# Kernel tuning notes

Hardware: AMD Instinct MI355X
Metric: run time of the kernel (lower is better)

## Reference

```python
import jax, jax.numpy as jnp
import numpy as np

N_PATCHES = 16
HID = 8
HEADS = 2
DH = HID // HEADS          # 4
L = 2                       # n_blocks
DIM = 10                    # betas.shape[0]
C = 3
S_DIM = 224
PS = S_DIM // N_PATCHES     # 14
INPUT_D = C * PS * PS       # 588
SEQ = N_PATCHES ** 2 + 1    # 257
MLP = 4 * HID               # 32
EPS = 1e-5


def _pos_embed():
    i = np.arange(SEQ, dtype=np.float64)[:, None]
    j = np.arange(HID, dtype=np.float64)[None, :]
    ang = i / 10000.0 ** ((j - (j % 2)) / HID)
    pe = np.where(j % 2 == 0, np.sin(ang), np.cos(ang))
    return jnp.asarray(pe, jnp.float32)


def setup_inputs() -> dict:
    key = jax.random.key(0)
    ks = jax.random.split(key, 24)
    g = lambda k, shape: (jax.random.normal(k, shape, jnp.float32) * 0.1)
    inp = {
        'images': jax.random.normal(ks[0], (512, C, S_DIM, S_DIM), jnp.float32),
        'inputs_labels': jax.random.randint(ks[1], (512,), 0, C),
        'Wm': g(ks[2], (INPUT_D, HID)), 'bm': g(ks[3], (HID,)),
        'cls_table': g(ks[4], (C, HID)),
        'pe': _pos_embed(),
        'ln1_g': jnp.ones((L, HID)), 'ln1_b': jnp.zeros((L, HID)),
        'Wq': g(ks[5], (L, HEADS, DH, DH)), 'bq': g(ks[6], (L, HEADS, DH)),
        'Wk': g(ks[7], (L, HEADS, DH, DH)), 'bk': g(ks[8], (L, HEADS, DH)),
        'Wv': g(ks[9], (L, HEADS, DH, DH)), 'bv': g(ks[10], (L, HEADS, DH)),
        'ln2_g': jnp.ones((L, HID)), 'ln2_b': jnp.zeros((L, HID)),
        'W1': g(ks[11], (L, HID, MLP)), 'b1': g(ks[12], (L, MLP)),
        'W2': g(ks[13], (L, MLP, HID)), 'b2': g(ks[14], (L, HID)),
        'Wf': g(ks[15], (HID, DIM)), 'bf': g(ks[16], (DIM,)),
    }
    return inp


def _layernorm(x, g, b):
    m = jnp.mean(x, axis=-1, keepdims=True)
    v = jnp.mean(jnp.square(x - m), axis=-1, keepdims=True)
    return (x - m) * jax.lax.rsqrt(v + EPS) * g + b


def _forward(images, inputs_labels, Wm, bm, cls_table, pe,
             ln1_g, ln1_b, Wq, bq, Wk, bk, Wv, bv,
             ln2_g, ln2_b, W1, b1, W2, b2, Wf, bf):
    n = images.shape[0]
    # patchify: [n,C,H,W] -> [n, n_patches^2, C*ps*ps]
    p = images.reshape(n, C, N_PATCHES, PS, N_PATCHES, PS)
    p = p.transpose(0, 2, 4, 1, 3, 5).reshape(n, N_PATCHES ** 2, INPUT_D)
    tokens = p @ Wm + bm                                # [n, 256, HID]
    cls = cls_table[inputs_labels][:, None, :]          # [n, 1, HID]
    x = jnp.concatenate([cls, tokens], axis=1) + pe[None]  # [n, SEQ, HID]
    scale = 1.0 / jnp.sqrt(jnp.float32(DH))
    for l in range(L):
        h = _layernorm(x, ln1_g[l], ln1_b[l]).reshape(n, SEQ, HEADS, DH)
        q = jnp.einsum('nshd,hde->nhse', h, Wq[l]) + bq[l][None, :, None, :]
        k = jnp.einsum('nshd,hde->nhse', h, Wk[l]) + bk[l][None, :, None, :]
        v = jnp.einsum('nshd,hde->nhse', h, Wv[l]) + bv[l][None, :, None, :]
        att = jax.nn.softmax(jnp.einsum('nhse,nhte->nhst', q, k) * scale, axis=-1)
        o = jnp.einsum('nhst,nhte->nhse', att, v)       # [n,H,S,DH]
        x = x + o.transpose(0, 2, 1, 3).reshape(n, SEQ, HID)
        h2 = _layernorm(x, ln2_g[l], ln2_b[l])
        x = x + jax.nn.gelu(h2 @ W1[l] + b1[l], approximate=False) @ W2[l] + b2[l]
    return x[:, 0] @ Wf + bf                            # [n, DIM]


def reference(images, inputs_labels, Wm, bm, cls_table, pe,
              ln1_g, ln1_b, Wq, bq, Wk, bk, Wv, bv,
              ln2_g, ln2_b, W1, b1, W2, b2, Wf, bf):
    return _forward(images, inputs_labels, Wm, bm, cls_table, pe,
                    ln1_g, ln1_b, Wq, bq, Wk, bk, Wv, bv,
                    ln2_g, ln2_b, W1, b1, W2, b2, Wf, bf)
```

## Files before the change

### kernel.cpp

```cpp
#include <hip/hip_runtime.h>

#define N_IMG_D 150528
#define CH_STRIDE 50176

__global__ __launch_bounds__(256) void k_patch_embed(
    const float* __restrict__ img, const float* __restrict__ Wm,
    const float* __restrict__ bm, const float* __restrict__ pe,
    float* __restrict__ xws)
{
    __shared__ __align__(16) float wmA[588 * 4];
    __shared__ __align__(16) float wmB[588 * 4];
    __shared__ __align__(16) float red[224 * 8];

    const int t = threadIdx.x;
    const int b = blockIdx.x;
    const int n = b >> 4, py = b & 15;

    for (int i = t; i < 1176; i += 256) {
        float4 w = reinterpret_cast<const float4*>(Wm)[i];
        float* dst = (i & 1) ? wmB : wmA;
        *reinterpret_cast<float4*>(dst + (i >> 1) * 4) = w;
    }
    __syncthreads();

    if (t < 224) {
        const int rp = t / 112;
        const int t1 = t - rp * 112;
        const int px = t1 / 7;
        const int j  = t1 - px * 7;
        const int col0 = 2 * j;
        const float* ib = img + (size_t)n * N_IMG_D + (py * 14) * 224 + px * 14 + col0;
        float a0=0,a1=0,a2=0,a3=0,a4=0,a5=0,a6=0,a7=0;
        int c = 0, r = rp;
        const float* wA = wmA + (rp * 14 + col0) * 4;
        const float* wB = wmB + (rp * 14 + col0) * 4;
        #pragma unroll
        for (int it = 0; it < 21; ++it) {
            const float2 v = *reinterpret_cast<const float2*>(ib + c * CH_STRIDE + r * 224);
            const float4 wa0 = *reinterpret_cast<const float4*>(wA);
            const float4 wa1 = *reinterpret_cast<const float4*>(wA + 4);
            const float4 wb0 = *reinterpret_cast<const float4*>(wB);
            const float4 wb1 = *reinterpret_cast<const float4*>(wB + 4);
            a0 += v.x * wa0.x + v.y * wa1.x;
            a1 += v.x * wa0.y + v.y * wa1.y;
            a2 += v.x * wa0.z + v.y * wa1.z;
            a3 += v.x * wa0.w + v.y * wa1.w;
            a4 += v.x * wb0.x + v.y * wb1.x;
            a5 += v.x * wb0.y + v.y * wb1.y;
            a6 += v.x * wb0.z + v.y * wb1.z;
            a7 += v.x * wb0.w + v.y * wb1.w;
            r += 2;
            if (r >= 14) { r -= 14; c += 1; }
            wA += 28 * 4; wB += 28 * 4;
        }
        *reinterpret_cast<float4*>(red + t * 8)     = make_float4(a0, a1, a2, a3);
        *reinterpret_cast<float4*>(red + t * 8 + 4) = make_float4(a4, a5, a6, a7);
    }
    __syncthreads();

    if (t < 128) {
        const int px = t >> 3, e = t & 7;
        float s = 0.f;
        #pragma unroll
        for (int rp = 0; rp < 2; ++rp) {
            #pragma unroll
            for (int j = 0; j < 7; ++j)
                s += red[(rp * 112 + px * 7 + j) * 8 + e];
        }
        const int row = 1 + py * 16 + px;
        s += bm[e] + pe[row * 8 + e];
        xws[((size_t)n * 257 + row) * 8 + e] = s;
    }
}

__global__ __launch_bounds__(576) void k_transformer(
    const float* __restrict__ xws, const int* __restrict__ labels,
    const float* __restrict__ cls_table, const float* __restrict__ pe,
    const float* __restrict__ ln1_g, const float* __restrict__ ln1_b,
    const float* __restrict__ Wq, const float* __restrict__ bq,
    const float* __restrict__ Wk, const float* __restrict__ bk,
    const float* __restrict__ Wv, const float* __restrict__ bv,
    const float* __restrict__ ln2_g, const float* __restrict__ ln2_b,
    const float* __restrict__ W1, const float* __restrict__ b1,
    const float* __restrict__ W2, const float* __restrict__ b2,
    const float* __restrict__ Wf, const float* __restrict__ bf,
    float* __restrict__ out)
{
    __shared__ __align__(16) float xb[257 * 9];
    __shared__ __align__(16) float hb[257 * 9];
    __shared__ __align__(16) float qb[2 * 257 * 4];
    __shared__ __align__(16) float kb[2 * 257 * 4];
    __shared__ __align__(16) float vb[2 * 257 * 4];
    __shared__ float wqs[64], wks[64], wvs[64];
    __shared__ float bqs[16], bks[16], bvs[16];
    __shared__ float w1s[512], b1s[64], w2s[512], b2s[16];

    const int t = threadIdx.x;
    const int n = blockIdx.x;
    const float* xn = xws + (size_t)n * 2056;

    for (int i = t; i < 64; i += 576) { wqs[i] = Wq[i]; wks[i] = Wk[i]; wvs[i] = Wv[i]; b1s[i] = b1[i]; }
    for (int i = t; i < 16; i += 576) { bqs[i] = bq[i]; bks[i] = bk[i]; bvs[i] = bv[i]; b2s[i] = b2[i]; }
    for (int i = t; i < 512; i += 576) { w1s[i] = W1[i]; w2s[i] = W2[i]; }

    if (t < 512) {
        float4 v = reinterpret_cast<const float4*>(xn)[t + 2];
        const int s = (t + 2) >> 1;
        const int e0 = (t & 1) ? 4 : 0;
        float* d = xb + s * 9 + e0;
        d[0] = v.x; d[1] = v.y; d[2] = v.z; d[3] = v.w;
    } else if (t < 520) {
        const int e = t - 512;
        xb[e] = cls_table[labels[n] * 8 + e] + pe[e];
    }
    __syncthreads();

    const float SC = 0.72134752044f;

    for (int l = 0; l < 2; ++l) {
        if (t < 257) {
            float v0[8]; float m = 0.f;
            #pragma unroll
            for (int e = 0; e < 8; ++e) { v0[e] = xb[t * 9 + e]; m += v0[e]; }
            m *= 0.125f;
            float var = 0.f;
            #pragma unroll
            for (int e = 0; e < 8; ++e) { float d = v0[e] - m; var += d * d; }
            var *= 0.125f;
            const float rs = rsqrtf(var + 1e-5f);
            const float* g = ln1_g + l * 8; const float* bb = ln1_b + l * 8;
            float ln[8];
            #pragma unroll
            for (int e = 0; e < 8; ++e) ln[e] = (v0[e] - m) * rs * g[e] + bb[e];

            #pragma unroll
            for (int h = 0; h < 2; ++h) {
                const int wb_ = (l * 2 + h);
                const float* wq = wqs + wb_ * 16; const float* bq_ = bqs + wb_ * 4;
                const float* wk = wks + wb_ * 16; const float* bk_ = bks + wb_ * 4;
                const float* wv = wvs + wb_ * 16; const float* bv_ = bvs + wb_ * 4;
                float qq[4], kk[4], vv[4];
                #pragma unroll
                for (int e = 0; e < 4; ++e) { qq[e] = bq_[e]; kk[e] = bk_[e]; vv[e] = bv_[e]; }
                #pragma unroll
                for (int d = 0; d < 4; ++d) {
                    const float hd = ln[h * 4 + d];
                    #pragma unroll
                    for (int e = 0; e < 4; ++e) {
                        qq[e] += hd * wq[d * 4 + e];
                        kk[e] += hd * wk[d * 4 + e];
                        vv[e] += hd * wv[d * 4 + e];
                    }
                }
                const int ri = (h * 257 + t) * 4;
                *reinterpret_cast<float4*>(qb + ri) =
                    make_float4(qq[0] * SC, qq[1] * SC, qq[2] * SC, qq[3] * SC);
                *reinterpret_cast<float4*>(kb + ri) = make_float4(kk[0], kk[1], kk[2], kk[3]);
                *reinterpret_cast<float4*>(vb + ri) = make_float4(vv[0], vv[1], vv[2], vv[3]);
            }
        }
        __syncthreads();

        if (t < 258) {
            const int h = (t >= 129) ? 1 : 0;
            const int j = t - 129 * h;
            const int s0 = j;
            const int s1 = j + 129;
            const bool has2 = (j < 128);
            const float4* qp = reinterpret_cast<const float4*>(qb) + h * 257;
            const float4* kp = reinterpret_cast<const float4*>(kb) + h * 257;
            const float4* vp = reinterpret_cast<const float4*>(vb) + h * 257;
            const float4 q0 = qp[s0];
            const float4 q1 = qp[has2 ? s1 : s0];

            float l0 = 0.f, o00 = 0.f, o01 = 0.f, o02 = 0.f, o03 = 0.f;
            float l1 = 0.f, o10 = 0.f, o11 = 0.f, o12 = 0.f, o13 = 0.f;
            #pragma unroll 4
            for (int tt = 0; tt < 257; ++tt) {
                const float4 kk = kp[tt];
                const float4 vv = vp[tt];
                const float d0 = q0.x * kk.x + q0.y * kk.y + q0.z * kk.z + q0.w * kk.w;
                const float d1 = q1.x * kk.x + q1.y * kk.y + q1.z * kk.z + q1.w * kk.w;
                const float p0 = exp2f(d0);
                const float p1 = exp2f(d1);
                l0 += p0; l1 += p1;
                o00 += p0 * vv.x; o01 += p0 * vv.y; o02 += p0 * vv.z; o03 += p0 * vv.w;
                o10 += p1 * vv.x; o11 += p1 * vv.y; o12 += p1 * vv.z; o13 += p1 * vv.w;
            }
            const float i0 = 1.0f / l0;
            float* xr0 = xb + s0 * 9 + h * 4;
            xr0[0] += o00 * i0; xr0[1] += o01 * i0; xr0[2] += o02 * i0; xr0[3] += o03 * i0;
            if (has2) {
                const float i1 = 1.0f / l1;
                float* xr1 = xb + s1 * 9 + h * 4;
                xr1[0] += o10 * i1; xr1[1] += o11 * i1; xr1[2] += o12 * i1; xr1[3] += o13 * i1;
            }
        }
        __syncthreads();

        if (t < 257) {
            float v0[8]; float m = 0.f;
            #pragma unroll
            for (int e = 0; e < 8; ++e) { v0[e] = xb[t * 9 + e]; m += v0[e]; }
            m *= 0.125f;
            float var = 0.f;
            #pragma unroll
            for (int e = 0; e < 8; ++e) { float d = v0[e] - m; var += d * d; }
            var *= 0.125f;
            const float rs = rsqrtf(var + 1e-5f);
            const float* g = ln2_g + l * 8; const float* bb = ln2_b + l * 8;
            #pragma unroll
            for (int e = 0; e < 8; ++e) hb[t * 9 + e] = (v0[e] - m) * rs * g[e] + bb[e];
        }
        __syncthreads();

        if (t < 257) {
            float hv[8];
            #pragma unroll
            for (int e = 0; e < 8; ++e) hv[e] = hb[t * 9 + e];
            float acc[8] = {0.f, 0.f, 0.f, 0.f, 0.f, 0.f, 0.f, 0.f};
            const float* w1 = w1s + l * 256; const float* bb1 = b1s + l * 32;
            const float* w2 = w2s + l * 256; const float* bb2 = b2s + l * 8;
            for (int u = 0; u < 32; ++u) {
                float a = bb1[u];
                #pragma unroll
                for (int e = 0; e < 8; ++e) a += hv[e] * w1[e * 32 + u];
                const float gl = 0.5f * a * (1.0f + erff(a * 0.70710678f));
                #pragma unroll
                for (int e = 0; e < 8; ++e) acc[e] += gl * w2[u * 8 + e];
            }
            #pragma unroll
            for (int e = 0; e < 8; ++e) xb[t * 9 + e] += acc[e] + bb2[e];
        }
        __syncthreads();
    }

    if (t < 10) {
        float a = bf[t];
        #pragma unroll
        for (int e = 0; e < 8; ++e) a += xb[e] * Wf[e * 10 + t];
        out[(size_t)n * 10 + t] = a;
    }
}

extern "C" void kernel_launch(void* const* d_in, const int* in_sizes, int n_in,
                              void* d_out, int out_size, void* d_ws, size_t ws_size,
                              hipStream_t stream) {
    const float* img    = (const float*)d_in[0];
    const int*   labels = (const int*)  d_in[1];
    const float* Wm     = (const float*)d_in[2];
    const float* bm     = (const float*)d_in[3];
    const float* cls    = (const float*)d_in[4];
    const float* pe     = (const float*)d_in[5];
    const float* ln1_g  = (const float*)d_in[6];
    const float* ln1_b  = (const float*)d_in[7];
    const float* Wq     = (const float*)d_in[8];
    const float* bq     = (const float*)d_in[9];
    const float* Wk     = (const float*)d_in[10];
    const float* bk     = (const float*)d_in[11];
    const float* Wv     = (const float*)d_in[12];
    const float* bv     = (const float*)d_in[13];
    const float* ln2_g  = (const float*)d_in[14];
    const float* ln2_b  = (const float*)d_in[15];
    const float* W1     = (const float*)d_in[16];
    const float* b1     = (const float*)d_in[17];
    const float* W2     = (const float*)d_in[18];
    const float* b2     = (const float*)d_in[19];
    const float* Wf     = (const float*)d_in[20];
    const float* bf     = (const float*)d_in[21];
    float* out = (float*)d_out;
    float* xws = (float*)d_ws;

    const int n = in_sizes[0] / N_IMG_D;
    k_patch_embed<<<n * 16, 256, 0, stream>>>(img, Wm, bm, pe, xws);
    k_transformer<<<n, 576, 0, stream>>>(xws, labels, cls, pe, ln1_g, ln1_b,
        Wq, bq, Wk, bk, Wv, bv, ln2_g, ln2_b, W1, b1, W2, b2, Wf, bf, out);
}
```

Baseline: 564.8 us.

## Fuse patch embedding into transformer kernel and retile attention to four queries per thread

Removes the separate patch-embedding kernel. Each transformer block now computes its own patch tokens: 512 threads each handle one patch and one half of the 21 rows, reading Wm directly from global memory, and the two halves are combined through shared memory. This drops the workspace round trip and one kernel launch. Attention is also remapped so 128 threads each process four queries, plus two threads for the last row, which reuses each K/V load across more queries but runs on far fewer active threads. The per-thread image reads in the fused embedding are strided, and with only 512 blocks the image-loading phase may be less well parallelised than the earlier 8192-block kernel.

```diff
diff --git a/kernel.cpp b/kernel.cpp
--- a/kernel.cpp
+++ b/kernel.cpp
@@ -3,78 +3,9 @@
 #define N_IMG_D 150528
 #define CH_STRIDE 50176
 
-__global__ __launch_bounds__(256) void k_patch_embed(
-    const float* __restrict__ img, const float* __restrict__ Wm,
-    const float* __restrict__ bm, const float* __restrict__ pe,
-    float* __restrict__ xws)
-{
-    __shared__ __align__(16) float wmA[588 * 4];
-    __shared__ __align__(16) float wmB[588 * 4];
-    __shared__ __align__(16) float red[224 * 8];
-
-    const int t = threadIdx.x;
-    const int b = blockIdx.x;
-    const int n = b >> 4, py = b & 15;
-
-    for (int i = t; i < 1176; i += 256) {
-        float4 w = reinterpret_cast<const float4*>(Wm)[i];
-        float* dst = (i & 1) ? wmB : wmA;
-        *reinterpret_cast<float4*>(dst + (i >> 1) * 4) = w;
-    }
-    __syncthreads();
-
-    if (t < 224) {
-        const int rp = t / 112;
-        const int t1 = t - rp * 112;
-        const int px = t1 / 7;
-        const int j  = t1 - px * 7;
-        const int col0 = 2 * j;
-        const float* ib = img + (size_t)n * N_IMG_D + (py * 14) * 224 + px * 14 + col0;
-        float a0=0,a1=0,a2=0,a3=0,a4=0,a5=0,a6=0,a7=0;
-        int c = 0, r = rp;
-        const float* wA = wmA + (rp * 14 + col0) * 4;
-        const float* wB = wmB + (rp * 14 + col0) * 4;
-        #pragma unroll
-        for (int it = 0; it < 21; ++it) {
-            const float2 v = *reinterpret_cast<const float2*>(ib + c * CH_STRIDE + r * 224);
-            const float4 wa0 = *reinterpret_cast<const float4*>(wA);
-            const float4 wa1 = *reinterpret_cast<const float4*>(wA + 4);
-            const float4 wb0 = *reinterpret_cast<const float4*>(wB);
-            const float4 wb1 = *reinterpret_cast<const float4*>(wB + 4);
-            a0 += v.x * wa0.x + v.y * wa1.x;
-            a1 += v.x * wa0.y + v.y * wa1.y;
-            a2 += v.x * wa0.z + v.y * wa1.z;
-            a3 += v.x * wa0.w + v.y * wa1.w;
-            a4 += v.x * wb0.x + v.y * wb1.x;
-            a5 += v.x * wb0.y + v.y * wb1.y;
-            a6 += v.x * wb0.z + v.y * wb1.z;
-            a7 += v.x * wb0.w + v.y * wb1.w;
-            r += 2;
-            if (r >= 14) { r -= 14; c += 1; }
-            wA += 28 * 4; wB += 28 * 4;
-        }
-        *reinterpret_cast<float4*>(red + t * 8)     = make_float4(a0, a1, a2, a3);
-        *reinterpret_cast<float4*>(red + t * 8 + 4) = make_float4(a4, a5, a6, a7);
-    }
-    __syncthreads();
-
-    if (t < 128) {
-        const int px = t >> 3, e = t & 7;
-        float s = 0.f;
-        #pragma unroll
-        for (int rp = 0; rp < 2; ++rp) {
-            #pragma unroll
-            for (int j = 0; j < 7; ++j)
-                s += red[(rp * 112 + px * 7 + j) * 8 + e];
-        }
-        const int row = 1 + py * 16 + px;
-        s += bm[e] + pe[row * 8 + e];
-        xws[((size_t)n * 257 + row) * 8 + e] = s;
-    }
-}
-
-__global__ __launch_bounds__(576) void k_transformer(
-    const float* __restrict__ xws, const int* __restrict__ labels,
+__global__ __launch_bounds__(576) void k_vit_fused(
+    const float* __restrict__ img, const int* __restrict__ labels,
+    const float* __restrict__ Wm, const float* __restrict__ bm,
     const float* __restrict__ cls_table, const float* __restrict__ pe,
     const float* __restrict__ ln1_g, const float* __restrict__ ln1_b,
     const float* __restrict__ Wq, const float* __restrict__ bq,
@@ -91,27 +22,54 @@
     __shared__ __align__(16) float qb[2 * 257 * 4];
     __shared__ __align__(16) float kb[2 * 257 * 4];
     __shared__ __align__(16) float vb[2 * 257 * 4];
+    __shared__ float red2[256 * 9];
     __shared__ float wqs[64], wks[64], wvs[64];
     __shared__ float bqs[16], bks[16], bvs[16];
     __shared__ float w1s[512], b1s[64], w2s[512], b2s[16];
 
     const int t = threadIdx.x;
     const int n = blockIdx.x;
-    const float* xn = xws + (size_t)n * 2056;
 
     for (int i = t; i < 64; i += 576) { wqs[i] = Wq[i]; wks[i] = Wk[i]; wvs[i] = Wv[i]; b1s[i] = b1[i]; }
     for (int i = t; i < 16; i += 576) { bqs[i] = bq[i]; bks[i] = bk[i]; bvs[i] = bv[i]; b2s[i] = b2[i]; }
     for (int i = t; i < 512; i += 576) { w1s[i] = W1[i]; w2s[i] = W2[i]; }
 
-    if (t < 512) {
-        float4 v = reinterpret_cast<const float4*>(xn)[t + 2];
-        const int s = (t + 2) >> 1;
-        const int e0 = (t & 1) ? 4 : 0;
-        float* d = xb + s * 9 + e0;
-        d[0] = v.x; d[1] = v.y; d[2] = v.z; d[3] = v.w;
+    const bool emb = (t < 512);
+    int half = 0, p = 0;
+    float acc[8] = {0.f, 0.f, 0.f, 0.f, 0.f, 0.f, 0.f, 0.f};
+    if (emb) {
+        half = __builtin_amdgcn_readfirstlane(t >> 8);
+        p = t & 255;
+        const int py = p >> 4, px = p & 15;
+        int c = half;
+        int r = half * 7;
+        const float* ib = img + (size_t)n * N_IMG_D + c * CH_STRIDE + (py * 14 + r) * 224 + px * 14;
+        const float* wrow = Wm + (c * 196 + r * 14) * 8;
+        for (int it = 0; it < 21; ++it) {
+            #pragma unroll 7
+            for (int col = 0; col < 14; ++col) {
+                const float v = ib[col];
+                const float* w = wrow + col * 8;
+                #pragma unroll
+                for (int e = 0; e < 8; ++e) acc[e] += v * w[e];
+            }
+            ++r; ib += 224; wrow += 112;
+            if (r == 14) { r = 0; ++c; ib += CH_STRIDE - 14 * 224; }
+        }
+        if (half) {
+            #pragma unroll
+            for (int e = 0; e < 8; ++e) red2[p * 9 + e] = acc[e];
+        }
     } else if (t < 520) {
         const int e = t - 512;
         xb[e] = cls_table[labels[n] * 8 + e] + pe[e];
+    }
+    __syncthreads();
+    if (emb && half == 0) {
+        const float* pr = pe + (p + 1) * 8;
+        #pragma unroll
+        for (int e = 0; e < 8; ++e)
+            xb[(p + 1) * 9 + e] = acc[e] + red2[p * 9 + e] + bm[e] + pr[e];
     }
     __syncthreads();
 
@@ -161,39 +119,65 @@
         }
         __syncthreads();
 
-        if (t < 258) {
-            const int h = (t >= 129) ? 1 : 0;
-            const int j = t - 129 * h;
-            const int s0 = j;
-            const int s1 = j + 129;
-            const bool has2 = (j < 128);
-            const float4* qp = reinterpret_cast<const float4*>(qb) + h * 257;
-            const float4* kp = reinterpret_cast<const float4*>(kb) + h * 257;
-            const float4* vp = reinterpret_cast<const float4*>(vb) + h * 257;
-            const float4 q0 = qp[s0];
-            const float4 q1 = qp[has2 ? s1 : s0];
-
-            float l0 = 0.f, o00 = 0.f, o01 = 0.f, o02 = 0.f, o03 = 0.f;
-            float l1 = 0.f, o10 = 0.f, o11 = 0.f, o12 = 0.f, o13 = 0.f;
-            #pragma unroll 4
-            for (int tt = 0; tt < 257; ++tt) {
-                const float4 kk = kp[tt];
-                const float4 vv = vp[tt];
-                const float d0 = q0.x * kk.x + q0.y * kk.y + q0.z * kk.z + q0.w * kk.w;
-                const float d1 = q1.x * kk.x + q1.y * kk.y + q1.z * kk.z + q1.w * kk.w;
-                const float p0 = exp2f(d0);
-                const float p1 = exp2f(d1);
-                l0 += p0; l1 += p1;
-                o00 += p0 * vv.x; o01 += p0 * vv.y; o02 += p0 * vv.z; o03 += p0 * vv.w;
-                o10 += p1 * vv.x; o11 += p1 * vv.y; o12 += p1 * vv.z; o13 += p1 * vv.w;
-            }
-            const float i0 = 1.0f / l0;
-            float* xr0 = xb + s0 * 9 + h * 4;
-            xr0[0] += o00 * i0; xr0[1] += o01 * i0; xr0[2] += o02 * i0; xr0[3] += o03 * i0;
-            if (has2) {
-                const float i1 = 1.0f / l1;
-                float* xr1 = xb + s1 * 9 + h * 4;
-                xr1[0] += o10 * i1; xr1[1] += o11 * i1; xr1[2] += o12 * i1; xr1[3] += o13 * i1;
+        if (t < 130) {
+            if (t < 128) {
+                const int h  = t >> 6;
+                const int j0 = t & 63;
+                const float4* qp = reinterpret_cast<const float4*>(qb) + h * 257;
+                const float4* kp = reinterpret_cast<const float4*>(kb) + h * 257;
+                const float4* vp = reinterpret_cast<const float4*>(vb) + h * 257;
+                const float4 q0 = qp[j0], q1 = qp[j0 + 64], q2 = qp[j0 + 128], q3 = qp[j0 + 192];
+                float l0 = 0.f, l1 = 0.f, l2 = 0.f, l3 = 0.f;
+                float4 o0 = {0,0,0,0}, o1 = {0,0,0,0}, o2 = {0,0,0,0}, o3 = {0,0,0,0};
+                #pragma unroll 2
+                for (int tt = 0; tt < 257; ++tt) {
+                    const float4 kk = kp[tt];
+                    const float4 vv = vp[tt];
+                    const float d0 = q0.x*kk.x + q0.y*kk.y + q0.z*kk.z + q0.w*kk.w;
+                    const float d1 = q1.x*kk.x + q1.y*kk.y + q1.z*kk.z + q1.w*kk.w;
+                    const float d2 = q2.x*kk.x + q2.y*kk.y + q2.z*kk.z + q2.w*kk.w;
+                    const float d3 = q3.x*kk.x + q3.y*kk.y + q3.z*kk.z + q3.w*kk.w;
+                    const float p0 = exp2f(d0), p1 = exp2f(d1), p2 = exp2f(d2), p3 = exp2f(d3);
+                    l0 += p0; l1 += p1; l2 += p2; l3 += p3;
+                    o0.x += p0*vv.x; o0.y += p0*vv.y; o0.z += p0*vv.z; o0.w += p0*vv.w;
+                    o1.x += p1*vv.x; o1.y += p1*vv.y; o1.z += p1*vv.z; o1.w += p1*vv.w;
+                    o2.x += p2*vv.x; o2.y += p2*vv.y; o2.z += p2*vv.z; o2.w += p2*vv.w;
+                    o3.x += p3*vv.x; o3.y += p3*vv.y; o3.z += p3*vv.z; o3.w += p3*vv.w;
+                }
+                {
+                    const float i0 = 1.0f / l0; float* xr = xb + (j0      ) * 9 + h * 4;
+                    xr[0] += o0.x*i0; xr[1] += o0.y*i0; xr[2] += o0.z*i0; xr[3] += o0.w*i0;
+                }
+                {
+                    const float i1 = 1.0f / l1; float* xr = xb + (j0 +  64) * 9 + h * 4;
+                    xr[0] += o1.x*i1; xr[1] += o1.y*i1; xr[2] += o1.z*i1; xr[3] += o1.w*i1;
+                }
+                {
+                    const float i2 = 1.0f / l2; float* xr = xb + (j0 + 128) * 9 + h * 4;
+                    xr[0] += o2.x*i2; xr[1] += o2.y*i2; xr[2] += o2.z*i2; xr[3] += o2.w*i2;
+                }
+                {
+                    const float i3 = 1.0f / l3; float* xr = xb + (j0 + 192) * 9 + h * 4;
+                    xr[0] += o3.x*i3; xr[1] += o3.y*i3; xr[2] += o3.z*i3; xr[3] += o3.w*i3;
+                }
+            } else {
+                const int h = t - 128;
+                const float4* qp = reinterpret_cast<const float4*>(qb) + h * 257;
+                const float4* kp = reinterpret_cast<const float4*>(kb) + h * 257;
+                const float4* vp = reinterpret_cast<const float4*>(vb) + h * 257;
+                const float4 q0 = qp[256];
+                float l0 = 0.f; float4 o0 = {0,0,0,0};
+                #pragma unroll 2
+                for (int tt = 0; tt < 257; ++tt) {
+                    const float4 kk = kp[tt];
+                    const float4 vv = vp[tt];
+                    const float d0 = q0.x*kk.x + q0.y*kk.y + q0.z*kk.z + q0.w*kk.w;
+                    const float p0 = exp2f(d0);
+                    l0 += p0;
+                    o0.x += p0*vv.x; o0.y += p0*vv.y; o0.z += p0*vv.z; o0.w += p0*vv.w;
+                }
+                const float i0 = 1.0f / l0; float* xr = xb + 256 * 9 + h * 4;
+                xr[0] += o0.x*i0; xr[1] += o0.y*i0; xr[2] += o0.z*i0; xr[3] += o0.w*i0;
             }
         }
         __syncthreads();
@@ -218,7 +202,7 @@
             float hv[8];
             #pragma unroll
             for (int e = 0; e < 8; ++e) hv[e] = hb[t * 9 + e];
-            float acc[8] = {0.f, 0.f, 0.f, 0.f, 0.f, 0.f, 0.f, 0.f};
+            float a8[8] = {0.f, 0.f, 0.f, 0.f, 0.f, 0.f, 0.f, 0.f};
             const float* w1 = w1s + l * 256; const float* bb1 = b1s + l * 32;
             const float* w2 = w2s + l * 256; const float* bb2 = b2s + l * 8;
             for (int u = 0; u < 32; ++u) {
@@ -227,10 +211,10 @@
                 for (int e = 0; e < 8; ++e) a += hv[e] * w1[e * 32 + u];
                 const float gl = 0.5f * a * (1.0f + erff(a * 0.70710678f));
                 #pragma unroll
-                for (int e = 0; e < 8; ++e) acc[e] += gl * w2[u * 8 + e];
-            }
-            #pragma unroll
-            for (int e = 0; e < 8; ++e) xb[t * 9 + e] += acc[e] + bb2[e];
+                for (int e = 0; e < 8; ++e) a8[e] += gl * w2[u * 8 + e];
+            }
+            #pragma unroll
+            for (int e = 0; e < 8; ++e) xb[t * 9 + e] += a8[e] + bb2[e];
         }
         __syncthreads();
     }
@@ -269,10 +253,9 @@
     const float* Wf     = (const float*)d_in[20];
     const float* bf     = (const float*)d_in[21];
     float* out = (float*)d_out;
-    float* xws = (float*)d_ws;
 
     const int n = in_sizes[0] / N_IMG_D;
-    k_patch_embed<<<n * 16, 256, 0, stream>>>(img, Wm, bm, pe, xws);
-    k_transformer<<<n, 576, 0, stream>>>(xws, labels, cls, pe, ln1_g, ln1_b,
-        Wq, bq, Wk, bk, Wv, bv, ln2_g, ln2_b, W1, b1, W2, b2, Wf, bf, out);
+    k_vit_fused<<<n, 576, 0, stream>>>(img, labels, Wm, bm, cls, pe,
+        ln1_g, ln1_b, Wq, bq, Wk, bk, Wv, bv, ln2_g, ln2_b,
+        W1, b1, W2, b2, Wf, bf, out);
 }
```

After: 630.0 us. 1.12x slower.

## Reuse patch-embed weight loads across four patches per thread

Applied to the files above, without the earlier changes.

The patch-embed kernel now has each thread cover the same column pair of four horizontally adjacent patches, so every shared-memory weight float4 load feeds four image float2 loads. Each thread keeps 32 accumulators and walks rows with a stride of 8 instead of 2. The reduction now sums 56 partials per output through a padded 33-stride shared buffer. This is meant to cut LDS weight traffic and raise memory-level parallelism on image reads, at the cost of more registers, a larger shared reduction buffer and an uneven split of 6 or 5 iterations across threads. The transformer-kernel edits are cosmetic only.

```diff
diff --git a/kernel.cpp b/kernel.cpp
--- a/kernel.cpp
+++ b/kernel.cpp
@@ -10,7 +10,7 @@
 {
     __shared__ __align__(16) float wmA[588 * 4];
     __shared__ __align__(16) float wmB[588 * 4];
-    __shared__ __align__(16) float red[224 * 8];
+    __shared__ float red[224 * 33];
 
     const int t = threadIdx.x;
     const int b = blockIdx.x;
@@ -24,52 +24,65 @@
     __syncthreads();
 
     if (t < 224) {
-        const int rp = t / 112;
-        const int t1 = t - rp * 112;
-        const int px = t1 / 7;
-        const int j  = t1 - px * 7;
+        const int s   = t / 28;
+        const int t1  = t - s * 28;
+        const int pg4 = t1 / 7;
+        const int j   = t1 - pg4 * 7;
         const int col0 = 2 * j;
-        const float* ib = img + (size_t)n * N_IMG_D + (py * 14) * 224 + px * 14 + col0;
-        float a0=0,a1=0,a2=0,a3=0,a4=0,a5=0,a6=0,a7=0;
-        int c = 0, r = rp;
-        const float* wA = wmA + (rp * 14 + col0) * 4;
-        const float* wB = wmB + (rp * 14 + col0) * 4;
-        #pragma unroll
-        for (int it = 0; it < 21; ++it) {
-            const float2 v = *reinterpret_cast<const float2*>(ib + c * CH_STRIDE + r * 224);
+        int c = 0, r = s;
+        const float* ib = img + (size_t)n * N_IMG_D + (py * 14 + r) * 224 + pg4 * 14 + col0;
+        const float* wA = wmA + (s * 14 + col0) * 4;
+        const float* wB = wmB + (s * 14 + col0) * 4;
+        float a[32];
+        #pragma unroll
+        for (int i = 0; i < 32; ++i) a[i] = 0.f;
+        const int iters = (s < 2) ? 6 : 5;
+        for (int it = 0; it < iters; ++it) {
+            const float2 v0 = *reinterpret_cast<const float2*>(ib);
+            const float2 v1 = *reinterpret_cast<const float2*>(ib + 56);
+            const float2 v2 = *reinterpret_cast<const float2*>(ib + 112);
+            const float2 v3 = *reinterpret_cast<const float2*>(ib + 168);
             const float4 wa0 = *reinterpret_cast<const float4*>(wA);
             const float4 wa1 = *reinterpret_cast<const float4*>(wA + 4);
             const float4 wb0 = *reinterpret_cast<const float4*>(wB);
             const float4 wb1 = *reinterpret_cast<const float4*>(wB + 4);
-            a0 += v.x * wa0.x + v.y * wa1.x;
-            a1 += v.x * wa0.y + v.y * wa1.y;
-            a2 += v.x * wa0.z + v.y * wa1.z;
-            a3 += v.x * wa0.w + v.y * wa1.w;
-            a4 += v.x * wb0.x + v.y * wb1.x;
-            a5 += v.x * wb0.y + v.y * wb1.y;
-            a6 += v.x * wb0.z + v.y * wb1.z;
-            a7 += v.x * wb0.w + v.y * wb1.w;
-            r += 2;
-            if (r >= 14) { r -= 14; c += 1; }
-            wA += 28 * 4; wB += 28 * 4;
-        }
-        *reinterpret_cast<float4*>(red + t * 8)     = make_float4(a0, a1, a2, a3);
-        *reinterpret_cast<float4*>(red + t * 8 + 4) = make_float4(a4, a5, a6, a7);
+            a[0]  += v0.x*wa0.x + v0.y*wa1.x;  a[1]  += v0.x*wa0.y + v0.y*wa1.y;
+            a[2]  += v0.x*wa0.z + v0.y*wa1.z;  a[3]  += v0.x*wa0.w + v0.y*wa1.w;
+            a[4]  += v0.x*wb0.x + v0.y*wb1.x;  a[5]  += v0.x*wb0.y + v0.y*wb1.y;
+            a[6]  += v0.x*wb0.z + v0.y*wb1.z;  a[7]  += v0.x*wb0.w + v0.y*wb1.w;
+            a[8]  += v1.x*wa0.x + v1.y*wa1.x;  a[9]  += v1.x*wa0.y + v1.y*wa1.y;
+            a[10] += v1.x*wa0.z + v1.y*wa1.z;  a[11] += v1.x*wa0.w + v1.y*wa1.w;
+            a[12] += v1.x*wb0.x + v1.y*wb1.x;  a[13] += v1.x*wb0.y + v1.y*wb1.y;
+            a[14] += v1.x*wb0.z + v1.y*wb1.z;  a[15] += v1.x*wb0.w + v1.y*wb1.w;
+            a[16] += v2.x*wa0.x + v2.y*wa1.x;  a[17] += v2.x*wa0.y + v2.y*wa1.y;
+            a[18] += v2.x*wa0.z + v2.y*wa1.z;  a[19] += v2.x*wa0.w + v2.y*wa1.w;
+            a[20] += v2.x*wb0.x + v2.y*wb1.x;  a[21] += v2.x*wb0.y + v2.y*wb1.y;
+            a[22] += v2.x*wb0.z + v2.y*wb1.z;  a[23] += v2.x*wb0.w + v2.y*wb1.w;
+            a[24] += v3.x*wa0.x + v3.y*wa1.x;  a[25] += v3.x*wa0.y + v3.y*wa1.y;
+            a[26] += v3.x*wa0.z + v3.y*wa1.z;  a[27] += v3.x*wa0.w + v3.y*wa1.w;
+            a[28] += v3.x*wb0.x + v3.y*wb1.x;  a[29] += v3.x*wb0.y + v3.y*wb1.y;
+            a[30] += v3.x*wb0.z + v3.y*wb1.z;  a[31] += v3.x*wb0.w + v3.y*wb1.w;
+            r += 8; ib += 8 * 224; wA += 448; wB += 448;
+            if (r >= 14) { r -= 14; ++c; ib += CH_STRIDE - 14 * 224; }
+        }
+        float* rd = red + t * 33;
+        #pragma unroll
+        for (int i = 0; i < 32; ++i) rd[i] = a[i];
     }
     __syncthreads();
 
     if (t < 128) {
-        const int px = t >> 3, e = t & 7;
-        float s = 0.f;
-        #pragma unroll
-        for (int rp = 0; rp < 2; ++rp) {
-            #pragma unroll
-            for (int j = 0; j < 7; ++j)
-                s += red[(rp * 112 + px * 7 + j) * 8 + e];
-        }
-        const int row = 1 + py * 16 + px;
-        s += bm[e] + pe[row * 8 + e];
-        xws[((size_t)n * 257 + row) * 8 + e] = s;
+        const int p = t >> 3, e = t & 7;
+        const int pg4 = p & 3, sub = p >> 2;
+        float sum = 0.f;
+        #pragma unroll
+        for (int q = 0; q < 56; ++q) {
+            const int s = q / 7, j = q - s * 7;
+            sum += red[(s * 28 + pg4 * 7 + j) * 33 + sub * 8 + e];
+        }
+        const int row = 1 + py * 16 + p;
+        sum += bm[e] + pe[row * 8 + e];
+        xws[((size_t)n * 257 + row) * 8 + e] = sum;
     }
 }
 
@@ -179,21 +192,21 @@
             for (int tt = 0; tt < 257; ++tt) {
                 const float4 kk = kp[tt];
                 const float4 vv = vp[tt];
-                const float d0 = q0.x * kk.x + q0.y * kk.y + q0.z * kk.z + q0.w * kk.w;
-                const float d1 = q1.x * kk.x + q1.y * kk.y + q1.z * kk.z + q1.w * kk.w;
+                const float d0 = q0.x*kk.x + q0.y*kk.y + q0.z*kk.z + q0.w*kk.w;
+                const float d1 = q1.x*kk.x + q1.y*kk.y + q1.z*kk.z + q1.w*kk.w;
                 const float p0 = exp2f(d0);
                 const float p1 = exp2f(d1);
                 l0 += p0; l1 += p1;
-                o00 += p0 * vv.x; o01 += p0 * vv.y; o02 += p0 * vv.z; o03 += p0 * vv.w;
-                o10 += p1 * vv.x; o11 += p1 * vv.y; o12 += p1 * vv.z; o13 += p1 * vv.w;
+                o00 += p0*vv.x; o01 += p0*vv.y; o02 += p0*vv.z; o03 += p0*vv.w;
+                o10 += p1*vv.x; o11 += p1*vv.y; o12 += p1*vv.z; o13 += p1*vv.w;
             }
             const float i0 = 1.0f / l0;
             float* xr0 = xb + s0 * 9 + h * 4;
-            xr0[0] += o00 * i0; xr0[1] += o01 * i0; xr0[2] += o02 * i0; xr0[3] += o03 * i0;
+            xr0[0] += o00*i0; xr0[1] += o01*i0; xr0[2] += o02*i0; xr0[3] += o03*i0;
             if (has2) {
                 const float i1 = 1.0f / l1;
                 float* xr1 = xb + s1 * 9 + h * 4;
-                xr1[0] += o10 * i1; xr1[1] += o11 * i1; xr1[2] += o12 * i1; xr1[3] += o13 * i1;
+                xr1[0] += o10*i1; xr1[1] += o11*i1; xr1[2] += o12*i1; xr1[3] += o13*i1;
             }
         }
         __syncthreads();
@@ -218,7 +231,7 @@
             float hv[8];
             #pragma unroll
             for (int e = 0; e < 8; ++e) hv[e] = hb[t * 9 + e];
-            float acc[8] = {0.f, 0.f, 0.f, 0.f, 0.f, 0.f, 0.f, 0.f};
+            float a8[8] = {0.f, 0.f, 0.f, 0.f, 0.f, 0.f, 0.f, 0.f};
             const float* w1 = w1s + l * 256; const float* bb1 = b1s + l * 32;
             const float* w2 = w2s + l * 256; const float* bb2 = b2s + l * 8;
             for (int u = 0; u < 32; ++u) {
@@ -227,10 +240,10 @@
                 for (int e = 0; e < 8; ++e) a += hv[e] * w1[e * 32 + u];
                 const float gl = 0.5f * a * (1.0f + erff(a * 0.70710678f));
                 #pragma unroll
-                for (int e = 0; e < 8; ++e) acc[e] += gl * w2[u * 8 + e];
-            }
-            #pragma unroll
-            for (int e = 0; e < 8; ++e) xb[t * 9 + e] += acc[e] + bb2[e];
+                for (int e = 0; e < 8; ++e) a8[e] += gl * w2[u * 8 + e];
+            }
+            #pragma unroll
+            for (int e = 0; e < 8; ++e) xb[t * 9 + e] += a8[e] + bb2[e];
         }
         __syncthreads();
     }
```

Measured after the change: 572.2 us. About the same (+1.3%).
